# Kernel tuning notes

Measured on AMD Instinct MI355X. Metric: run time of the kernel, lower is better.

Reference implementation:

```python
import jax, jax.numpy as jnp
import numpy as np

N, L, D = 8192, 50, 64          # batch nodes, history length, embed_dim
NUM_ITEMS, NUM_ATTRS, NUM_FAM = 50000, 100000, 100000


def setup_inputs() -> dict:
    key = jax.random.key(0)
    ks = jax.random.split(key, 12)
    scale = 0.05
    return {
        "nodes": jax.random.randint(ks[0], (N,), 0, NUM_ITEMS),
        "history_va": jax.random.randint(ks[1], (N, L), 0, NUM_ATTRS),
        "history_af": jax.random.randint(ks[2], (N, L), 0, NUM_FAM),
        "v2e_w": jax.random.normal(ks[3], (NUM_ITEMS, D), jnp.float32) * scale,
        "a2e_w": jax.random.normal(ks[4], (NUM_ATTRS, D), jnp.float32) * scale,
        "f2e_w": jax.random.normal(ks[5], (NUM_FAM, D), jnp.float32) * scale,
        "W1": jax.random.normal(ks[6], (3 * D, D), jnp.float32) * scale,
        "b1": jnp.zeros((D,), jnp.float32),
        "W2": jax.random.normal(ks[7], (D, D), jnp.float32) * scale,
        "b2": jnp.zeros((D,), jnp.float32),
        "w3": jax.random.normal(ks[8], (D, 1), jnp.float32) * scale,
        "b3": jnp.zeros((1,), jnp.float32),
    }


def reference(nodes, history_va, history_af, v2e_w, a2e_w, f2e_w,
              W1, b1, W2, b2, w3, b3):
    # Batched form of the per-node loop (va=True branch).
    e_va = a2e_w[history_va]                       # [N, L, D] gathered attr embeds
    e_af = f2e_w[history_af]                       # [N, L, D] gathered famous embeds
    va_rep = v2e_w[nodes]                          # [N, D]    target item embed
    rep = jnp.broadcast_to(va_rep[:, None, :], e_va.shape)
    x = jnp.concatenate([e_va, rep, e_af], axis=-1)  # [N, L, 3D]
    h = jax.nn.relu(x @ W1 + b1)                   # [N, L, D]
    h = jax.nn.relu(h @ W2 + b2)                   # [N, L, D]
    scores = (h @ w3 + b3)[..., 0]                 # [N, L]
    att = jax.nn.softmax(scores, axis=1)           # softmax over history dim
    # e_va.T @ att per node  ==  weighted sum over history
    return jnp.einsum("nld,nl->nd", e_va, att)     # [N, D]
```

## Files before the change

### kernel.cpp

```cpp
#include <hip/hip_runtime.h>
#include <hip/hip_bf16.h>

typedef __bf16 bf16x8 __attribute__((ext_vector_type(8)));
typedef __bf16 bf16x4 __attribute__((ext_vector_type(4)));
typedef float  f32x4  __attribute__((ext_vector_type(4)));

#define HL   50
#define DD   64
#define NPB  2
#define MR   112
#define MT   7
#define XSS  136

__global__ __launch_bounds__(256, 5) void va_agg_kernel(
    const int*   __restrict__ nodes,
    const int*   __restrict__ hva,
    const int*   __restrict__ haf,
    const float* __restrict__ v2e,
    const float* __restrict__ a2e,
    const float* __restrict__ f2e,
    const float* __restrict__ W1,
    const float* __restrict__ b1,
    const float* __restrict__ W2,
    const float* __restrict__ b2,
    const float* __restrict__ w3,
    float*       __restrict__ out)
{
    __shared__ __bf16 xs[MR * XSS];
    __shared__ float  pbuf[4 * MR];

    const int tid  = threadIdx.x;
    const int w    = tid >> 6;
    const int lane = tid & 63;
    const int lq   = lane & 15;
    const int quad = lane >> 4;
    const int col  = w * 16 + lq;
    const int n0   = blockIdx.x * NPB;

    {
        const int* hb = hva + n0 * HL;
        const int* fb = haf + n0 * HL;
        #pragma unroll
        for (int i = 0; i < 13; ++i) {
            int t = i * 256 + tid;
            if (t < NPB * HL * 2 * 16) {
                int r = t >> 4, q = t & 15;
                bool va = (r < NPB * HL);
                int gr = va ? r : r - NPB * HL;
                int idx = va ? hb[gr] : fb[gr];
                const float* src = (va ? a2e : f2e) + (size_t)idx * DD + q * 4;
                float4 v = *(const float4*)src;
                bf16x4 pk = {(__bf16)v.x, (__bf16)v.y, (__bf16)v.z, (__bf16)v.w};
                *(bf16x4*)&xs[gr * XSS + (va ? 0 : DD) + q * 4] = pk;
            }
        }
    }

    bf16x8 repf[2];
    #pragma unroll
    for (int t = 0; t < 2; ++t)
        #pragma unroll
        for (int j = 0; j < 8; ++j) repf[t][j] = (__bf16)0.f;
    if (lq < NPB) {
        int nd = nodes[n0 + lq];
        const float* rp = v2e + (size_t)nd * DD;
        #pragma unroll
        for (int t = 0; t < 2; ++t) {
            float4 v0 = *(const float4*)(rp + t * 32 + quad * 8);
            float4 v1 = *(const float4*)(rp + t * 32 + quad * 8 + 4);
            repf[t] = (bf16x8){(__bf16)v0.x, (__bf16)v0.y, (__bf16)v0.z, (__bf16)v0.w,
                               (__bf16)v1.x, (__bf16)v1.y, (__bf16)v1.z, (__bf16)v1.w};
        }
    }

    bf16x8 b1f[4], b1u[2], b2f[2];
    #pragma unroll
    for (int t = 0; t < 4; ++t)
        #pragma unroll
        for (int j = 0; j < 8; ++j) {
            int keff = t * 32 + quad * 8 + j;
            int krow = (keff < 64) ? keff : keff + 64;
            b1f[t][j] = (__bf16)W1[krow * 64 + col];
        }
    #pragma unroll
    for (int t = 0; t < 2; ++t)
        #pragma unroll
        for (int j = 0; j < 8; ++j) {
            b1u[t][j] = (__bf16)W1[(64 + t * 32 + quad * 8 + j) * 64 + col];
            b2f[t][j] = (__bf16)W2[(t * 32 + quad * 8 + j) * 64 + col];
        }
    const float w3c = w3[col];
    const float b1c = b1[col];
    const float b2c = b2[col];

    f32x4 rb = {0.f, 0.f, 0.f, 0.f};
    #pragma unroll
    for (int t = 0; t < 2; ++t)
        rb = __builtin_amdgcn_mfma_f32_16x16x32_bf16(repf[t], b1u[t], rb, 0, 0, 0);
    const float bias0 = __shfl(rb[0], lq) + b1c;
    const float bias1 = __shfl(rb[1], lq) + b1c;

    __syncthreads();

    f32x4 acc[MT];
    #pragma unroll
    for (int mt = 0; mt < MT; ++mt)
        #pragma unroll
        for (int r = 0; r < 4; ++r) {
            int gr = mt * 16 + quad * 4 + r;
            acc[mt][r] = (gr >= HL) ? bias1 : bias0;
        }
    #pragma unroll
    for (int t = 0; t < 4; ++t)
        #pragma unroll
        for (int mt = 0; mt < MT; ++mt) {
            bf16x8 a = *(const bf16x8*)&xs[(mt * 16 + lq) * XSS + t * 32 + quad * 8];
            acc[mt] = __builtin_amdgcn_mfma_f32_16x16x32_bf16(a, b1f[t], acc[mt], 0, 0, 0);
        }
    __syncthreads();
    #pragma unroll
    for (int mt = 0; mt < MT; ++mt)
        #pragma unroll
        for (int r = 0; r < 4; ++r) {
            int gr = mt * 16 + quad * 4 + r;
            xs[gr * XSS + DD + col] = (__bf16)fmaxf(acc[mt][r], 0.f);
        }
    __syncthreads();

    f32x4 a2[MT];
    #pragma unroll
    for (int mt = 0; mt < MT; ++mt) a2[mt] = (f32x4){b2c, b2c, b2c, b2c};
    #pragma unroll
    for (int t = 0; t < 2; ++t)
        #pragma unroll
        for (int mt = 0; mt < MT; ++mt) {
            bf16x8 a = *(const bf16x8*)&xs[(mt * 16 + lq) * XSS + DD + t * 32 + quad * 8];
            a2[mt] = __builtin_amdgcn_mfma_f32_16x16x32_bf16(a, b2f[t], a2[mt], 0, 0, 0);
        }
    #pragma unroll
    for (int mt = 0; mt < MT; ++mt) {
        float p0 = fmaxf(a2[mt][0], 0.f) * w3c;
        float p1 = fmaxf(a2[mt][1], 0.f) * w3c;
        float p2 = fmaxf(a2[mt][2], 0.f) * w3c;
        float p3 = fmaxf(a2[mt][3], 0.f) * w3c;
        #pragma unroll
        for (int m = 1; m < 16; m <<= 1) {
            p0 += __shfl_xor(p0, m);
            p1 += __shfl_xor(p1, m);
            p2 += __shfl_xor(p2, m);
            p3 += __shfl_xor(p3, m);
        }
        if (lq == 0) {
            int rowb = mt * 16 + quad * 4;
            pbuf[w * MR + rowb + 0] = p0;
            pbuf[w * MR + rowb + 1] = p1;
            pbuf[w * MR + rowb + 2] = p2;
            pbuf[w * MR + rowb + 3] = p3;
        }
    }
    __syncthreads();

    const int n  = w & 1;
    const int lh = w >> 1;
    float att;
    {
        float s = -3.0e38f;
        if (lane < HL) {
            int gr = n * HL + lane;
            s = pbuf[gr] + pbuf[MR + gr] + pbuf[2 * MR + gr] + pbuf[3 * MR + gr];
        }
        float mx = s;
        #pragma unroll
        for (int m = 1; m < 64; m <<= 1) mx = fmaxf(mx, __shfl_xor(mx, m));
        float e = (lane < HL) ? __expf(s - mx) : 0.f;
        float sm = e;
        #pragma unroll
        for (int m = 1; m < 64; m <<= 1) sm += __shfl_xor(sm, m);
        att = e / sm;
    }

    {
        float o = 0.f;
        const int lb = lh * 25;
        #pragma unroll
        for (int i = 0; i < 25; ++i) {
            int l = lb + i;
            float av = __shfl(att, l);
            o = fmaf(av, (float)xs[(n * HL + l) * XSS + lane], o);
        }
        float* op = (float*)&xs[(100 + w) * XSS + DD];
        op[lane] = o;
    }
    __syncthreads();
    if (w < NPB) {
        const float* p0 = (const float*)&xs[(100 + w) * XSS + DD];
        const float* p1 = (const float*)&xs[(100 + w + 2) * XSS + DD];
        out[(size_t)(n0 + w) * DD + lane] = p0[lane] + p1[lane];
    }
}

extern "C" void kernel_launch(void* const* d_in, const int* in_sizes, int n_in,
                              void* d_out, int out_size, void* d_ws, size_t ws_size,
                              hipStream_t stream) {
    const int*   nodes = (const int*)d_in[0];
    const int*   hva   = (const int*)d_in[1];
    const int*   haf   = (const int*)d_in[2];
    const float* v2e   = (const float*)d_in[3];
    const float* a2e   = (const float*)d_in[4];
    const float* f2e   = (const float*)d_in[5];
    const float* W1    = (const float*)d_in[6];
    const float* b1    = (const float*)d_in[7];
    const float* W2    = (const float*)d_in[8];
    const float* b2    = (const float*)d_in[9];
    const float* w3    = (const float*)d_in[10];
    float* out = (float*)d_out;

    const int N = in_sizes[0];
    const int blocks = N / NPB;
    va_agg_kernel<<<blocks, 256, 0, stream>>>(nodes, hva, haf, v2e, a2e, f2e,
                                              W1, b1, W2, b2, w3, out);
}
```

Before: 174.4 us.

## Make blocks persistent over four node pairs with register-prefetched gathers

Each block now processes four node pairs in a loop instead of one, so the W1/W2 weight fragments are loaded and converted once per block rather than per pair. The embedding gathers for the next pair are issued into registers (split into two phases) while the current pair's MFMA and softmax work runs, hiding global-memory gather latency. The cost is higher register pressure (launch bounds lowered from 5 to 4 waves) and a quarter of the grid size, which reduces occupancy and parallelism across CUs.

```diff
diff --git a/kernel.cpp b/kernel.cpp
--- a/kernel.cpp
+++ b/kernel.cpp
@@ -8,11 +8,12 @@
 #define HL   50
 #define DD   64
 #define NPB  2
+#define ITER 4
 #define MR   112
 #define MT   7
 #define XSS  136
 
-__global__ __launch_bounds__(256, 5) void va_agg_kernel(
+__global__ __launch_bounds__(256, 4) void va_agg_kernel(
     const int*   __restrict__ nodes,
     const int*   __restrict__ hva,
     const int*   __restrict__ haf,
@@ -35,43 +36,75 @@
     const int lq   = lane & 15;
     const int quad = lane >> 4;
     const int col  = w * 16 + lq;
-    const int n0   = blockIdx.x * NPB;
-
-    {
+    const int pairBase = blockIdx.x * ITER;
+
+    float4 pfa[7];
+    float4 pfb[6];
+    float4 rr[4];
+
+    auto prefA = [&](int pair) {
+        const int n0 = pair * NPB;
         const int* hb = hva + n0 * HL;
         const int* fb = haf + n0 * HL;
         #pragma unroll
-        for (int i = 0; i < 13; ++i) {
-            int t = i * 256 + tid;
+        for (int i = 0; i < 7; ++i) {
+            int t = i * 256 + tid, r = t >> 4, q = t & 15;
+            bool va = (r < NPB * HL);
+            int gr = va ? r : r - NPB * HL;
+            int idx = va ? hb[gr] : fb[gr];
+            pfa[i] = *(const float4*)((va ? a2e : f2e) + (size_t)idx * DD + q * 4);
+        }
+    };
+    auto prefB = [&](int pair) {
+        const int n0 = pair * NPB;
+        const int* hb = hva + n0 * HL;
+        const int* fb = haf + n0 * HL;
+        #pragma unroll
+        for (int i = 0; i < 6; ++i) {
+            int t = (i + 7) * 256 + tid;
             if (t < NPB * HL * 2 * 16) {
                 int r = t >> 4, q = t & 15;
                 bool va = (r < NPB * HL);
                 int gr = va ? r : r - NPB * HL;
                 int idx = va ? hb[gr] : fb[gr];
-                const float* src = (va ? a2e : f2e) + (size_t)idx * DD + q * 4;
-                float4 v = *(const float4*)src;
+                pfb[i] = *(const float4*)((va ? a2e : f2e) + (size_t)idx * DD + q * 4);
+            }
+        }
+        if (lq < NPB) {
+            int nd = nodes[n0 + lq];
+            const float* rp = v2e + (size_t)nd * DD;
+            rr[0] = *(const float4*)(rp + quad * 8);
+            rr[1] = *(const float4*)(rp + quad * 8 + 4);
+            rr[2] = *(const float4*)(rp + 32 + quad * 8);
+            rr[3] = *(const float4*)(rp + 32 + quad * 8 + 4);
+        }
+    };
+    auto storeAll = [&]() {
+        #pragma unroll
+        for (int i = 0; i < 7; ++i) {
+            int t = i * 256 + tid, r = t >> 4, q = t & 15;
+            bool va = (r < NPB * HL);
+            int gr = va ? r : r - NPB * HL;
+            float4 v = pfa[i];
+            bf16x4 pk = {(__bf16)v.x, (__bf16)v.y, (__bf16)v.z, (__bf16)v.w};
+            *(bf16x4*)&xs[gr * XSS + (va ? 0 : DD) + q * 4] = pk;
+        }
+        #pragma unroll
+        for (int i = 0; i < 6; ++i) {
+            int t = (i + 7) * 256 + tid;
+            if (t < NPB * HL * 2 * 16) {
+                int r = t >> 4, q = t & 15;
+                bool va = (r < NPB * HL);
+                int gr = va ? r : r - NPB * HL;
+                float4 v = pfb[i];
                 bf16x4 pk = {(__bf16)v.x, (__bf16)v.y, (__bf16)v.z, (__bf16)v.w};
                 *(bf16x4*)&xs[gr * XSS + (va ? 0 : DD) + q * 4] = pk;
             }
         }
-    }
-
-    bf16x8 repf[2];
-    #pragma unroll
-    for (int t = 0; t < 2; ++t)
-        #pragma unroll
-        for (int j = 0; j < 8; ++j) repf[t][j] = (__bf16)0.f;
-    if (lq < NPB) {
-        int nd = nodes[n0 + lq];
-        const float* rp = v2e + (size_t)nd * DD;
-        #pragma unroll
-        for (int t = 0; t < 2; ++t) {
-            float4 v0 = *(const float4*)(rp + t * 32 + quad * 8);
-            float4 v1 = *(const float4*)(rp + t * 32 + quad * 8 + 4);
-            repf[t] = (bf16x8){(__bf16)v0.x, (__bf16)v0.y, (__bf16)v0.z, (__bf16)v0.w,
-                               (__bf16)v1.x, (__bf16)v1.y, (__bf16)v1.z, (__bf16)v1.w};
-        }
-    }
+    };
+
+    prefA(pairBase);
+    prefB(pairBase);
 
     bf16x8 b1f[4], b1u[2], b2f[2];
     #pragma unroll
@@ -93,109 +126,128 @@
     const float b1c = b1[col];
     const float b2c = b2[col];
 
-    f32x4 rb = {0.f, 0.f, 0.f, 0.f};
-    #pragma unroll
-    for (int t = 0; t < 2; ++t)
-        rb = __builtin_amdgcn_mfma_f32_16x16x32_bf16(repf[t], b1u[t], rb, 0, 0, 0);
-    const float bias0 = __shfl(rb[0], lq) + b1c;
-    const float bias1 = __shfl(rb[1], lq) + b1c;
-
-    __syncthreads();
-
-    f32x4 acc[MT];
-    #pragma unroll
-    for (int mt = 0; mt < MT; ++mt)
-        #pragma unroll
-        for (int r = 0; r < 4; ++r) {
-            int gr = mt * 16 + quad * 4 + r;
-            acc[mt][r] = (gr >= HL) ? bias1 : bias0;
-        }
-    #pragma unroll
-    for (int t = 0; t < 4; ++t)
+    for (int it = 0; it < ITER; ++it) {
+        storeAll();
+        bf16x8 repf[2];
+        #pragma unroll
+        for (int t = 0; t < 2; ++t) {
+            float4 v0 = rr[2 * t], v1 = rr[2 * t + 1];
+            repf[t] = (bf16x8){(__bf16)v0.x, (__bf16)v0.y, (__bf16)v0.z, (__bf16)v0.w,
+                               (__bf16)v1.x, (__bf16)v1.y, (__bf16)v1.z, (__bf16)v1.w};
+        }
+        if (lq >= NPB)
+            #pragma unroll
+            for (int t = 0; t < 2; ++t)
+                #pragma unroll
+                for (int j = 0; j < 8; ++j) repf[t][j] = (__bf16)0.f;
+        __syncthreads();
+
+        if (it + 1 < ITER) prefA(pairBase + it + 1);
+
+        f32x4 rb = {0.f, 0.f, 0.f, 0.f};
+        #pragma unroll
+        for (int t = 0; t < 2; ++t)
+            rb = __builtin_amdgcn_mfma_f32_16x16x32_bf16(repf[t], b1u[t], rb, 0, 0, 0);
+        const float bias0 = __shfl(rb[0], lq) + b1c;
+        const float bias1 = __shfl(rb[1], lq) + b1c;
+
+        f32x4 acc[MT];
+        #pragma unroll
+        for (int mt = 0; mt < MT; ++mt)
+            #pragma unroll
+            for (int r = 0; r < 4; ++r) {
+                int gr = mt * 16 + quad * 4 + r;
+                acc[mt][r] = (gr >= HL) ? bias1 : bias0;
+            }
+        #pragma unroll
+        for (int t = 0; t < 4; ++t)
+            #pragma unroll
+            for (int mt = 0; mt < MT; ++mt) {
+                bf16x8 a = *(const bf16x8*)&xs[(mt * 16 + lq) * XSS + t * 32 + quad * 8];
+                acc[mt] = __builtin_amdgcn_mfma_f32_16x16x32_bf16(a, b1f[t], acc[mt], 0, 0, 0);
+            }
+        __syncthreads();
+        #pragma unroll
+        for (int mt = 0; mt < MT; ++mt)
+            #pragma unroll
+            for (int r = 0; r < 4; ++r) {
+                int gr = mt * 16 + quad * 4 + r;
+                xs[gr * XSS + DD + col] = (__bf16)fmaxf(acc[mt][r], 0.f);
+            }
+        __syncthreads();
+
+        f32x4 a2[MT];
+        #pragma unroll
+        for (int mt = 0; mt < MT; ++mt) a2[mt] = (f32x4){b2c, b2c, b2c, b2c};
+        #pragma unroll
+        for (int t = 0; t < 2; ++t)
+            #pragma unroll
+            for (int mt = 0; mt < MT; ++mt) {
+                bf16x8 a = *(const bf16x8*)&xs[(mt * 16 + lq) * XSS + DD + t * 32 + quad * 8];
+                a2[mt] = __builtin_amdgcn_mfma_f32_16x16x32_bf16(a, b2f[t], a2[mt], 0, 0, 0);
+            }
         #pragma unroll
         for (int mt = 0; mt < MT; ++mt) {
-            bf16x8 a = *(const bf16x8*)&xs[(mt * 16 + lq) * XSS + t * 32 + quad * 8];
-            acc[mt] = __builtin_amdgcn_mfma_f32_16x16x32_bf16(a, b1f[t], acc[mt], 0, 0, 0);
-        }
-    __syncthreads();
-    #pragma unroll
-    for (int mt = 0; mt < MT; ++mt)
-        #pragma unroll
-        for (int r = 0; r < 4; ++r) {
-            int gr = mt * 16 + quad * 4 + r;
-            xs[gr * XSS + DD + col] = (__bf16)fmaxf(acc[mt][r], 0.f);
-        }
-    __syncthreads();
-
-    f32x4 a2[MT];
-    #pragma unroll
-    for (int mt = 0; mt < MT; ++mt) a2[mt] = (f32x4){b2c, b2c, b2c, b2c};
-    #pragma unroll
-    for (int t = 0; t < 2; ++t)
-        #pragma unroll
-        for (int mt = 0; mt < MT; ++mt) {
-            bf16x8 a = *(const bf16x8*)&xs[(mt * 16 + lq) * XSS + DD + t * 32 + quad * 8];
-            a2[mt] = __builtin_amdgcn_mfma_f32_16x16x32_bf16(a, b2f[t], a2[mt], 0, 0, 0);
-        }
-    #pragma unroll
-    for (int mt = 0; mt < MT; ++mt) {
-        float p0 = fmaxf(a2[mt][0], 0.f) * w3c;
-        float p1 = fmaxf(a2[mt][1], 0.f) * w3c;
-        float p2 = fmaxf(a2[mt][2], 0.f) * w3c;
-        float p3 = fmaxf(a2[mt][3], 0.f) * w3c;
-        #pragma unroll
-        for (int m = 1; m < 16; m <<= 1) {
-            p0 += __shfl_xor(p0, m);
-            p1 += __shfl_xor(p1, m);
-            p2 += __shfl_xor(p2, m);
-            p3 += __shfl_xor(p3, m);
-        }
-        if (lq == 0) {
-            int rowb = mt * 16 + quad * 4;
-            pbuf[w * MR + rowb + 0] = p0;
-            pbuf[w * MR + rowb + 1] = p1;
-            pbuf[w * MR + rowb + 2] = p2;
-            pbuf[w * MR + rowb + 3] = p3;
-        }
-    }
-    __syncthreads();
-
-    const int n  = w & 1;
-    const int lh = w >> 1;
-    float att;
-    {
-        float s = -3.0e38f;
-        if (lane < HL) {
-            int gr = n * HL + lane;
-            s = pbuf[gr] + pbuf[MR + gr] + pbuf[2 * MR + gr] + pbuf[3 * MR + gr];
-        }
-        float mx = s;
-        #pragma unroll
-        for (int m = 1; m < 64; m <<= 1) mx = fmaxf(mx, __shfl_xor(mx, m));
-        float e = (lane < HL) ? __expf(s - mx) : 0.f;
-        float sm = e;
-        #pragma unroll
-        for (int m = 1; m < 64; m <<= 1) sm += __shfl_xor(sm, m);
-        att = e / sm;
-    }
-
-    {
-        float o = 0.f;
-        const int lb = lh * 25;
-        #pragma unroll
-        for (int i = 0; i < 25; ++i) {
-            int l = lb + i;
-            float av = __shfl(att, l);
-            o = fmaf(av, (float)xs[(n * HL + l) * XSS + lane], o);
-        }
-        float* op = (float*)&xs[(100 + w) * XSS + DD];
-        op[lane] = o;
-    }
-    __syncthreads();
-    if (w < NPB) {
-        const float* p0 = (const float*)&xs[(100 + w) * XSS + DD];
-        const float* p1 = (const float*)&xs[(100 + w + 2) * XSS + DD];
-        out[(size_t)(n0 + w) * DD + lane] = p0[lane] + p1[lane];
+            float p0 = fmaxf(a2[mt][0], 0.f) * w3c;
+            float p1 = fmaxf(a2[mt][1], 0.f) * w3c;
+            float p2 = fmaxf(a2[mt][2], 0.f) * w3c;
+            float p3 = fmaxf(a2[mt][3], 0.f) * w3c;
+            #pragma unroll
+            for (int m = 1; m < 16; m <<= 1) {
+                p0 += __shfl_xor(p0, m);
+                p1 += __shfl_xor(p1, m);
+                p2 += __shfl_xor(p2, m);
+                p3 += __shfl_xor(p3, m);
+            }
+            if (lq == 0) {
+                int rowb = mt * 16 + quad * 4;
+                pbuf[w * MR + rowb + 0] = p0;
+                pbuf[w * MR + rowb + 1] = p1;
+                pbuf[w * MR + rowb + 2] = p2;
+                pbuf[w * MR + rowb + 3] = p3;
+            }
+        }
+        __syncthreads();
+
+        if (it + 1 < ITER) prefB(pairBase + it + 1);
+
+        const int n  = w & 1;
+        const int lh = w >> 1;
+        float att;
+        {
+            float s = -3.0e38f;
+            if (lane < HL) {
+                int gr = n * HL + lane;
+                s = pbuf[gr] + pbuf[MR + gr] + pbuf[2 * MR + gr] + pbuf[3 * MR + gr];
+            }
+            float mx = s;
+            #pragma unroll
+            for (int m = 1; m < 64; m <<= 1) mx = fmaxf(mx, __shfl_xor(mx, m));
+            float e = (lane < HL) ? __expf(s - mx) : 0.f;
+            float sm = e;
+            #pragma unroll
+            for (int m = 1; m < 64; m <<= 1) sm += __shfl_xor(sm, m);
+            att = e / sm;
+        }
+
+        {
+            float o = 0.f;
+            const int lb = lh * 25;
+            #pragma unroll
+            for (int i = 0; i < 25; ++i) {
+                int l = lb + i;
+                float av = __shfl(att, l);
+                o = fmaf(av, (float)xs[(n * HL + l) * XSS + lane], o);
+            }
+            float* op = (float*)&xs[(100 + w) * XSS + DD];
+            op[lane] = o;
+        }
+        __syncthreads();
+        if (w < NPB) {
+            const float* p0 = (const float*)&xs[(100 + w) * XSS + DD];
+            const float* p1 = (const float*)&xs[(100 + w + 2) * XSS + DD];
+            out[(size_t)((pairBase + it) * NPB + w) * DD + lane] = p0[lane] + p1[lane];
+        }
     }
 }
 
@@ -216,7 +268,7 @@
     float* out = (float*)d_out;
 
     const int N = in_sizes[0];
-    const int blocks = N / NPB;
+    const int blocks = N / (NPB * ITER);
     va_agg_kernel<<<blocks, 256, 0, stream>>>(nodes, hva, haf, v2e, a2e, f2e,
                                               W1, b1, W2, b2, w3, out);
 }
```

Measured after the change: 346.6 us. +98.8%, slower.
